# Kernel optimization log

Measured on AMD Instinct MI355X. Metric: run time of the kernel, lower is better.

The kernel has to match this reference:

```python
import jax, jax.numpy as jnp
import numpy as np

B = 16384          # batch size
NUM_NEG = 4
N = 1 + NUM_NEG    # items per row (pos + negs)
D = 128            # embedding_dim
F = 4              # num_factors
FS = D // F        # factor_size = 32
TD = 384           # bert_text_dim
NU = 100000        # num_users
NI = 100000        # num_items
HID = 150          # text MLP hidden
M = 2              # num_modalities


def _linear_init(k, fan_out, fan_in):
    bound = 1.0 / np.sqrt(fan_in)
    return jax.random.uniform(k, (fan_out, fan_in), jnp.float32, -bound, bound)


def setup_inputs() -> dict:
    key = jax.random.key(0)
    ks = jax.random.split(key, 12)
    batch = jax.random.randint(ks[0], (B, 1 + N), 0, NU)          # col0=user, cols1..5=items
    text = jax.random.normal(ks[1], (B, N, TD), dtype=jnp.float32)
    user_table = jax.random.normal(ks[2], (NU, D), dtype=jnp.float32)
    item_table = jax.random.normal(ks[3], (NI, D), dtype=jnp.float32)
    w1 = _linear_init(ks[4], HID, TD)
    b1 = jax.random.uniform(ks[5], (HID,), jnp.float32, -1/np.sqrt(TD), 1/np.sqrt(TD))
    w2 = _linear_init(ks[6], D, HID)
    b2 = jax.random.uniform(ks[7], (D,), jnp.float32, -1/np.sqrt(HID), 1/np.sqrt(HID))
    # per-factor attention MLPs, stacked over the F factors (all same size here)
    aw1 = jax.random.uniform(ks[8], (F, M, 3 * FS), jnp.float32, -1/np.sqrt(3*FS), 1/np.sqrt(3*FS))
    ab1 = jax.random.uniform(ks[9], (F, M), jnp.float32, -1/np.sqrt(3*FS), 1/np.sqrt(3*FS))
    aw2 = jax.random.uniform(ks[10], (F, M, M), jnp.float32, -1/np.sqrt(M), 1/np.sqrt(M))
    return dict(batch=batch, text=text, user_table=user_table, item_table=item_table,
                w1=w1, b1=b1, w2=w2, b2=b2, aw1=aw1, ab1=ab1, aw2=aw2)


def _leaky_relu(x):
    return jnp.where(x > 0, x, 0.01 * x)


def reference(batch, text, user_table, item_table, w1, b1, w2, b2, aw1, ab1, aw2):
    # text MLP: Linear -> LeakyReLU -> Linear -> LeakyReLU
    te = _leaky_relu(_leaky_relu(text @ w1.T + b1) @ w2.T + b2)   # [B,N,D]

    users = batch[:, 0]
    items = batch[:, 1:]
    u = user_table[users]                                          # [B,D]
    ie = item_table[items]                                         # [B,N,D]

    # split into F factors of size FS (vectorized over factor dim)
    uf = jnp.broadcast_to(u[:, None, :], ie.shape).reshape(B, N, F, FS)
    itf = ie.reshape(B, N, F, FS)
    tf = te.reshape(B, N, F, FS)

    cat = jnp.concatenate([uf, itf, tf], axis=-1)                  # [B,N,F,3*FS]
    nrm = jnp.linalg.norm(cat, axis=-1, keepdims=True)
    cat = cat / jnp.maximum(nrm, 1e-12)                            # F.normalize(dim=-1)

    h = jnp.tanh(jnp.einsum('bnfk,fmk->bnfm', cat, aw1) + ab1)     # [B,N,F,M]
    logits = jnp.einsum('bnfm,fom->bnfo', h, aw2)                  # [B,N,F,M]
    # torch nn.Softmax() with dim=None on a 3D tensor -> softmax over dim 0 (batch)
    attn = jax.nn.softmax(logits, axis=0)

    r_ui = attn[..., 0] * jax.nn.softplus(jnp.sum(uf * itf, axis=-1))  # [B,N,F]
    r_ut = attn[..., 1] * jax.nn.softplus(jnp.sum(uf * tf, axis=-1))   # [B,N,F]
    ratings = jnp.sum(r_ui + r_ut, axis=-1)                        # [B,N], sum over factors
    return ratings
```

## Files before the change

### kernel.cpp

```cpp
#include <hip/hip_runtime.h>
#include <hip/hip_bf16.h>

#define TDIM 384
#define HID 150
#define DD 128
#define ROWS 81920
#define RT 64

typedef __attribute__((ext_vector_type(8))) short short8;
typedef __attribute__((ext_vector_type(4))) float f32x4;

#define SMEM_BYTES 33792

__device__ __forceinline__ float lrelu(float x) { return x > 0.f ? x : 0.01f * x; }
__device__ __forceinline__ float softplusf(float x) {
    return fmaxf(x, 0.f) + log1pf(expf(-fabsf(x)));
}

__device__ __forceinline__ short8 pack8(const float4 a, const float4 b) {
    union { short8 s; __hip_bfloat16 h[8]; } u;
    u.h[0] = __float2bfloat16(a.x); u.h[1] = __float2bfloat16(a.y);
    u.h[2] = __float2bfloat16(a.z); u.h[3] = __float2bfloat16(a.w);
    u.h[4] = __float2bfloat16(b.x); u.h[5] = __float2bfloat16(b.y);
    u.h[6] = __float2bfloat16(b.z); u.h[7] = __float2bfloat16(b.w);
    return u.s;
}

__global__ __launch_bounds__(256)
void prep_w(const float* __restrict__ w1, const float* __restrict__ w2,
            short8* __restrict__ w1f, short8* __restrict__ w2f)
{
    const int idx = blockIdx.x * 256 + threadIdx.x;
    union { short8 s; __hip_bfloat16 h[8]; } u;
    if (idx < 7680) {
        const int kt = idx / 640, c = idx % 640;
        const int col = c >> 2, q = c & 3;
        const int k = kt * 32 + q * 8;
#pragma unroll
        for (int j = 0; j < 8; ++j)
            u.h[j] = __float2bfloat16(col < HID ? w1[(size_t)col * TDIM + k + j] : 0.f);
        w1f[idx] = u.s;
    } else if (idx < 10240) {
        const int i2 = idx - 7680;
        const int kt = i2 / 512, c = i2 % 512;
        const int col = c >> 2, q = c & 3;
        const int k = kt * 32 + q * 8;
#pragma unroll
        for (int j = 0; j < 8; ++j)
            u.h[j] = __float2bfloat16((k + j) < HID ? w2[(size_t)col * HID + k + j] : 0.f);
        w2f[i2] = u.s;
    }
}

__global__ __launch_bounds__(256, 4)
void fused_main(const int* __restrict__ batch,
                const float* __restrict__ text,
                const float* __restrict__ user_table,
                const float* __restrict__ item_table,
                const short8* __restrict__ w1f,
                const float* __restrict__ b1,
                const short8* __restrict__ w2f,
                const float* __restrict__ b2,
                const float* __restrict__ aw1,
                const float* __restrict__ ab1,
                const float* __restrict__ aw2,
                float* __restrict__ expp,
                float* __restrict__ Sglob)
{
    __shared__ __align__(16) unsigned char smem[SMEM_BYTES];
    __shared__ __align__(8) float red[512];
    __hip_bfloat16* Hs = (__hip_bfloat16*)(smem);
    float*          Ts = (float*)(smem);

    const int t    = threadIdx.x;
    const int r0   = blockIdx.x * RT;
    const int lane = t & 63;
    const int wv   = t >> 6;
    const int m16  = lane & 15;
    const int quad = lane >> 4;
    const int wr   = (wv & 1) * 32;
    const int wc   = (wv >> 1) * 80;
    const int wc2  = (wv >> 1) * 64;

    const int p3row = t >> 2;
    const int p3f   = t & 3;
    const int gr    = r0 + p3row;
    const int bb    = gr / 5;
    const int nn    = gr - bb * 5;
    const int uid   = batch[bb * 6];
    const int iid   = batch[bb * 6 + 1 + nn];

    const float* ta  = text + (size_t)(r0 + wr + m16) * TDIM;
    const float* tb  = ta + 16 * TDIM;
    const int    ko0 = quad * 8;
    const int w1base = (wc + m16) * 4 + quad;

    f32x4 acc1[2][5];
#pragma unroll
    for (int i = 0; i < 2; ++i)
#pragma unroll
        for (int j = 0; j < 5; ++j) acc1[i][j] = (f32x4){0.f, 0.f, 0.f, 0.f};

    float4 pA[2][4];
#pragma unroll
    for (int k = 0; k < 2; ++k) {
        pA[k][0] = *(const float4*)(ta + k * 32 + ko0);
        pA[k][1] = *(const float4*)(ta + k * 32 + ko0 + 4);
        pA[k][2] = *(const float4*)(tb + k * 32 + ko0);
        pA[k][3] = *(const float4*)(tb + k * 32 + ko0 + 4);
    }

#pragma unroll
    for (int kt = 0; kt < 12; ++kt) {
        const int p = kt & 1;
        short8 bw[5];
#pragma unroll
        for (int tj = 0; tj < 5; ++tj)
            bw[tj] = w1f[kt * 640 + w1base + tj * 64];
        const short8 a0 = pack8(pA[p][0], pA[p][1]);
        const short8 a1 = pack8(pA[p][2], pA[p][3]);
        if (kt < 10) {
            const int ko = (kt + 2) * 32 + ko0;
            pA[p][0] = *(const float4*)(ta + ko);
            pA[p][1] = *(const float4*)(ta + ko + 4);
            pA[p][2] = *(const float4*)(tb + ko);
            pA[p][3] = *(const float4*)(tb + ko + 4);
        }
#pragma unroll
        for (int tj = 0; tj < 5; ++tj) {
            acc1[0][tj] = __builtin_amdgcn_mfma_f32_16x16x32_bf16(a0, bw[tj], acc1[0][tj], 0, 0, 0);
            acc1[1][tj] = __builtin_amdgcn_mfma_f32_16x16x32_bf16(a1, bw[tj], acc1[1][tj], 0, 0, 0);
        }
    }

#pragma unroll
    for (int tj = 0; tj < 5; ++tj) {
        const int col = wc + tj * 16 + m16;
        const float bv = (col < HID) ? b1[col] : 0.f;
#pragma unroll
        for (int ti = 0; ti < 2; ++ti) {
#pragma unroll
            for (int r = 0; r < 4; ++r) {
                const int row = wr + ti * 16 + quad * 4 + r;
                float v = lrelu(acc1[ti][tj][r] + bv);
                if (col >= HID) v = 0.f;
                Hs[row * 168 + col] = __float2bfloat16(v);
            }
        }
    }
    __syncthreads();

    f32x4 acc2[2][4];
#pragma unroll
    for (int i = 0; i < 2; ++i)
#pragma unroll
        for (int j = 0; j < 4; ++j) acc2[i][j] = (f32x4){0.f, 0.f, 0.f, 0.f};

    const __hip_bfloat16* h0p = Hs + (wr + m16) * 168 + ko0;
    const __hip_bfloat16* h1p = h0p + 16 * 168;
    const int w2base = (wc2 + m16) * 4 + quad;

#pragma unroll
    for (int kt = 0; kt < 5; ++kt) {
        short8 bw[4];
#pragma unroll
        for (int tj = 0; tj < 4; ++tj)
            bw[tj] = w2f[kt * 512 + w2base + tj * 64];
        const short8 a0 = *(const short8*)(h0p + kt * 32);
        const short8 a1 = *(const short8*)(h1p + kt * 32);
#pragma unroll
        for (int tj = 0; tj < 4; ++tj) {
            acc2[0][tj] = __builtin_amdgcn_mfma_f32_16x16x32_bf16(a0, bw[tj], acc2[0][tj], 0, 0, 0);
            acc2[1][tj] = __builtin_amdgcn_mfma_f32_16x16x32_bf16(a1, bw[tj], acc2[1][tj], 0, 0, 0);
        }
    }
    __syncthreads();

#pragma unroll
    for (int tj = 0; tj < 4; ++tj) {
        const int col = wc2 + tj * 16 + m16;
        const float bv = b2[col];
#pragma unroll
        for (int ti = 0; ti < 2; ++ti) {
#pragma unroll
            for (int r = 0; r < 4; ++r) {
                const int row = wr + ti * 16 + quad * 4 + r;
                Ts[row * 132 + col] = lrelu(acc2[ti][tj][r] + bv);
            }
        }
    }

    const float* up = user_table + (size_t)uid * DD + p3f * 32;
    const float* ip = item_table + (size_t)iid * DD + p3f * 32;
    float4 ur[8], er[8];
#pragma unroll
    for (int q = 0; q < 8; ++q) {
        ur[q] = *(const float4*)(up + q * 4);
        er[q] = *(const float4*)(ip + q * 4);
    }
    __syncthreads();

    {
        const float* tp  = Ts + p3row * 132 + p3f * 32;
        const float* a1p = aw1 + p3f * 2 * 96;

        float ss = 0.f, z0 = 0.f, z1 = 0.f, sui = 0.f, sut = 0.f;
#pragma unroll
        for (int q = 0; q < 8; ++q) {
            const float4 u4 = ur[q];
            const float4 e4 = er[q];
            const float4 t4 = *(const float4*)(tp + q * 4);
            const float4 a00 = *(const float4*)(a1p + q * 4);
            const float4 a01 = *(const float4*)(a1p + 32 + q * 4);
            const float4 a02 = *(const float4*)(a1p + 64 + q * 4);
            const float4 a10 = *(const float4*)(a1p + 96 + q * 4);
            const float4 a11 = *(const float4*)(a1p + 128 + q * 4);
            const float4 a12 = *(const float4*)(a1p + 160 + q * 4);
            const float uu[4] = {u4.x, u4.y, u4.z, u4.w};
            const float ee[4] = {e4.x, e4.y, e4.z, e4.w};
            const float tt[4] = {t4.x, t4.y, t4.z, t4.w};
            const float w00[4] = {a00.x, a00.y, a00.z, a00.w};
            const float w01[4] = {a01.x, a01.y, a01.z, a01.w};
            const float w02[4] = {a02.x, a02.y, a02.z, a02.w};
            const float w10[4] = {a10.x, a10.y, a10.z, a10.w};
            const float w11[4] = {a11.x, a11.y, a11.z, a11.w};
            const float w12[4] = {a12.x, a12.y, a12.z, a12.w};
#pragma unroll
            for (int c = 0; c < 4; ++c) {
                const float u = uu[c], e = ee[c], x = tt[c];
                ss  = fmaf(u, u, ss); ss = fmaf(e, e, ss); ss = fmaf(x, x, ss);
                z0  = fmaf(u, w00[c], z0);
                z0  = fmaf(e, w01[c], z0);
                z0  = fmaf(x, w02[c], z0);
                z1  = fmaf(u, w10[c], z1);
                z1  = fmaf(e, w11[c], z1);
                z1  = fmaf(x, w12[c], z1);
                sui = fmaf(u, e, sui);
                sut = fmaf(u, x, sut);
            }
        }
        const float inv = 1.f / fmaxf(sqrtf(ss), 1e-12f);
        const float h0 = tanhf(fmaf(z0, inv, ab1[p3f * 2 + 0]));
        const float h1 = tanhf(fmaf(z1, inv, ab1[p3f * 2 + 1]));
        const float l0 = fmaf(h0, aw2[p3f * 4 + 0], h1 * aw2[p3f * 4 + 1]);
        const float l1 = fmaf(h0, aw2[p3f * 4 + 2], h1 * aw2[p3f * 4 + 3]);
        const float e0 = expf(l0), e1 = expf(l1);
        const float pui = softplusf(sui), put = softplusf(sut);
        *(float4*)&expp[((size_t)gr * 4 + p3f) * 4] = make_float4(e0, e1, pui, put);
        *(float2*)&red[p3row * 8 + p3f * 2] = make_float2(e0, e1);
    }
    __syncthreads();

    if (t < 40) {
        const int j   = t & 7;
        const int nn0 = t >> 3;
        int r = nn0 - (r0 % 5);
        if (r < 0) r += 5;
        float s = 0.f;
        for (; r < RT; r += 5) s += red[r * 8 + j];
        atomicAdd(&Sglob[t * 32], s);
    }
}

__global__ void finalize(const float* __restrict__ expp,
                         const float* __restrict__ Sglob,
                         float* __restrict__ out)
{
    const int gr = blockIdx.x * 256 + threadIdx.x;
    if (gr >= ROWS) return;
    const int b = gr / 5;
    const int n = gr - b * 5;
    float r = 0.f;
#pragma unroll
    for (int f = 0; f < 4; ++f) {
        const float4 v = *(const float4*)&expp[((size_t)gr * 4 + f) * 4];
        const float S0 = Sglob[(n * 8 + f * 2 + 0) * 32];
        const float S1 = Sglob[(n * 8 + f * 2 + 1) * 32];
        r += v.x / S0 * v.z + v.y / S1 * v.w;
    }
    out[gr] = r;
}

extern "C" void kernel_launch(void* const* d_in, const int* in_sizes, int n_in,
                              void* d_out, int out_size, void* d_ws, size_t ws_size,
                              hipStream_t stream)
{
    (void)in_sizes; (void)n_in; (void)out_size; (void)ws_size;
    const int*   batch      = (const int*)d_in[0];
    const float* text       = (const float*)d_in[1];
    const float* user_table = (const float*)d_in[2];
    const float* item_table = (const float*)d_in[3];
    const float* w1         = (const float*)d_in[4];
    const float* b1         = (const float*)d_in[5];
    const float* w2         = (const float*)d_in[6];
    const float* b2         = (const float*)d_in[7];
    const float* aw1        = (const float*)d_in[8];
    const float* ab1        = (const float*)d_in[9];
    const float* aw2        = (const float*)d_in[10];
    float* out = (float*)d_out;

    char* ws = (char*)d_ws;
    short8* w1f   = (short8*)ws;
    short8* w2f   = (short8*)(ws + 122880);
    float*  expp  = (float*)(ws + 163840);
    float*  Sglob = (float*)(ws + 163840 + (size_t)ROWS * 16 * 4);

    hipMemsetAsync(Sglob, 0, 40 * 32 * sizeof(float), stream);
    prep_w<<<40, 256, 0, stream>>>(w1, w2, w1f, w2f);
    fused_main<<<ROWS / RT, 256, 0, stream>>>(batch, text, user_table, item_table,
                                              w1f, b1, w2f, b2, aw1, ab1, aw2,
                                              expp, Sglob);
    finalize<<<(ROWS + 255) / 256, 256, 0, stream>>>(expp, Sglob, out);
}
```

Before: 352.2 us.

## Halve row tile, split per-factor work across lane pairs, replicate atomic sums

Shrinks the row tile from 64 to 32 so each wave does one 16-row MFMA strip, which halves accumulator registers and shared memory and raises launch bounds to 8 blocks per CU. The per-factor attention stage is split across two lanes per factor and combined with xor shuffles, so the 256 threads cover the smaller tile. Softmax denominator atomics are spread over 8 replicas to reduce contention, and finalize now reduces those replicas once into shared memory. The trade-off is twice as many blocks, with more redundant weight-fragment loads per row and more atomics overall.

```diff
diff --git a/kernel.cpp b/kernel.cpp
--- a/kernel.cpp
+++ b/kernel.cpp
@@ -5,12 +5,12 @@
 #define HID 150
 #define DD 128
 #define ROWS 81920
-#define RT 64
+#define RT 32
 
 typedef __attribute__((ext_vector_type(8))) short short8;
 typedef __attribute__((ext_vector_type(4))) float f32x4;
 
-#define SMEM_BYTES 33792
+#define SMEM_BYTES 16896
 
 __device__ __forceinline__ float lrelu(float x) { return x > 0.f ? x : 0.01f * x; }
 __device__ __forceinline__ float softplusf(float x) {
@@ -52,7 +52,7 @@
     }
 }
 
-__global__ __launch_bounds__(256, 4)
+__global__ __launch_bounds__(256, 8)
 void fused_main(const int* __restrict__ batch,
                 const float* __restrict__ text,
                 const float* __restrict__ user_table,
@@ -68,7 +68,7 @@
                 float* __restrict__ Sglob)
 {
     __shared__ __align__(16) unsigned char smem[SMEM_BYTES];
-    __shared__ __align__(8) float red[512];
+    __shared__ __align__(8) float red[RT * 8];
     __hip_bfloat16* Hs = (__hip_bfloat16*)(smem);
     float*          Ts = (float*)(smem);
 
@@ -78,36 +78,30 @@
     const int wv   = t >> 6;
     const int m16  = lane & 15;
     const int quad = lane >> 4;
-    const int wr   = (wv & 1) * 32;
+    const int wr   = (wv & 1) * 16;
     const int wc   = (wv >> 1) * 80;
     const int wc2  = (wv >> 1) * 64;
 
-    const int p3row = t >> 2;
-    const int p3f   = t & 3;
+    const int p3row = t >> 3;
+    const int p3f   = (t >> 1) & 3;
+    const int half  = t & 1;
     const int gr    = r0 + p3row;
     const int bb    = gr / 5;
     const int nn    = gr - bb * 5;
-    const int uid   = batch[bb * 6];
-    const int iid   = batch[bb * 6 + 1 + nn];
 
     const float* ta  = text + (size_t)(r0 + wr + m16) * TDIM;
-    const float* tb  = ta + 16 * TDIM;
     const int    ko0 = quad * 8;
     const int w1base = (wc + m16) * 4 + quad;
 
-    f32x4 acc1[2][5];
-#pragma unroll
-    for (int i = 0; i < 2; ++i)
-#pragma unroll
-        for (int j = 0; j < 5; ++j) acc1[i][j] = (f32x4){0.f, 0.f, 0.f, 0.f};
-
-    float4 pA[2][4];
+    f32x4 acc1[5];
+#pragma unroll
+    for (int j = 0; j < 5; ++j) acc1[j] = (f32x4){0.f, 0.f, 0.f, 0.f};
+
+    float4 pA[2][2];
 #pragma unroll
     for (int k = 0; k < 2; ++k) {
         pA[k][0] = *(const float4*)(ta + k * 32 + ko0);
         pA[k][1] = *(const float4*)(ta + k * 32 + ko0 + 4);
-        pA[k][2] = *(const float4*)(tb + k * 32 + ko0);
-        pA[k][3] = *(const float4*)(tb + k * 32 + ko0 + 4);
     }
 
 #pragma unroll
@@ -118,19 +112,14 @@
         for (int tj = 0; tj < 5; ++tj)
             bw[tj] = w1f[kt * 640 + w1base + tj * 64];
         const short8 a0 = pack8(pA[p][0], pA[p][1]);
-        const short8 a1 = pack8(pA[p][2], pA[p][3]);
         if (kt < 10) {
             const int ko = (kt + 2) * 32 + ko0;
             pA[p][0] = *(const float4*)(ta + ko);
             pA[p][1] = *(const float4*)(ta + ko + 4);
-            pA[p][2] = *(const float4*)(tb + ko);
-            pA[p][3] = *(const float4*)(tb + ko + 4);
-        }
-#pragma unroll
-        for (int tj = 0; tj < 5; ++tj) {
-            acc1[0][tj] = __builtin_amdgcn_mfma_f32_16x16x32_bf16(a0, bw[tj], acc1[0][tj], 0, 0, 0);
-            acc1[1][tj] = __builtin_amdgcn_mfma_f32_16x16x32_bf16(a1, bw[tj], acc1[1][tj], 0, 0, 0);
-        }
+        }
+#pragma unroll
+        for (int tj = 0; tj < 5; ++tj)
+            acc1[tj] = __builtin_amdgcn_mfma_f32_16x16x32_bf16(a0, bw[tj], acc1[tj], 0, 0, 0);
     }
 
 #pragma unroll
@@ -138,26 +127,20 @@
         const int col = wc + tj * 16 + m16;
         const float bv = (col < HID) ? b1[col] : 0.f;
 #pragma unroll
-        for (int ti = 0; ti < 2; ++ti) {
-#pragma unroll
-            for (int r = 0; r < 4; ++r) {
-                const int row = wr + ti * 16 + quad * 4 + r;
-                float v = lrelu(acc1[ti][tj][r] + bv);
-                if (col >= HID) v = 0.f;
-                Hs[row * 168 + col] = __float2bfloat16(v);
-            }
-        }
-    }
-    __syncthreads();
-
-    f32x4 acc2[2][4];
-#pragma unroll
-    for (int i = 0; i < 2; ++i)
-#pragma unroll
-        for (int j = 0; j < 4; ++j) acc2[i][j] = (f32x4){0.f, 0.f, 0.f, 0.f};
+        for (int r = 0; r < 4; ++r) {
+            const int row = wr + quad * 4 + r;
+            float v = lrelu(acc1[tj][r] + bv);
+            if (col >= HID) v = 0.f;
+            Hs[row * 168 + col] = __float2bfloat16(v);
+        }
+    }
+    __syncthreads();
+
+    f32x4 acc2[4];
+#pragma unroll
+    for (int j = 0; j < 4; ++j) acc2[j] = (f32x4){0.f, 0.f, 0.f, 0.f};
 
     const __hip_bfloat16* h0p = Hs + (wr + m16) * 168 + ko0;
-    const __hip_bfloat16* h1p = h0p + 16 * 168;
     const int w2base = (wc2 + m16) * 4 + quad;
 
 #pragma unroll
@@ -167,12 +150,9 @@
         for (int tj = 0; tj < 4; ++tj)
             bw[tj] = w2f[kt * 512 + w2base + tj * 64];
         const short8 a0 = *(const short8*)(h0p + kt * 32);
-        const short8 a1 = *(const short8*)(h1p + kt * 32);
-#pragma unroll
-        for (int tj = 0; tj < 4; ++tj) {
-            acc2[0][tj] = __builtin_amdgcn_mfma_f32_16x16x32_bf16(a0, bw[tj], acc2[0][tj], 0, 0, 0);
-            acc2[1][tj] = __builtin_amdgcn_mfma_f32_16x16x32_bf16(a1, bw[tj], acc2[1][tj], 0, 0, 0);
-        }
+#pragma unroll
+        for (int tj = 0; tj < 4; ++tj)
+            acc2[tj] = __builtin_amdgcn_mfma_f32_16x16x32_bf16(a0, bw[tj], acc2[tj], 0, 0, 0);
     }
     __syncthreads();
 
@@ -181,32 +161,31 @@
         const int col = wc2 + tj * 16 + m16;
         const float bv = b2[col];
 #pragma unroll
-        for (int ti = 0; ti < 2; ++ti) {
-#pragma unroll
-            for (int r = 0; r < 4; ++r) {
-                const int row = wr + ti * 16 + quad * 4 + r;
-                Ts[row * 132 + col] = lrelu(acc2[ti][tj][r] + bv);
-            }
-        }
-    }
-
-    const float* up = user_table + (size_t)uid * DD + p3f * 32;
-    const float* ip = item_table + (size_t)iid * DD + p3f * 32;
-    float4 ur[8], er[8];
-#pragma unroll
-    for (int q = 0; q < 8; ++q) {
+        for (int r = 0; r < 4; ++r) {
+            const int row = wr + quad * 4 + r;
+            Ts[row * 132 + col] = lrelu(acc2[tj][r] + bv);
+        }
+    }
+
+    const int uid = batch[bb * 6];
+    const int iid = batch[bb * 6 + 1 + nn];
+    const float* up = user_table + (size_t)uid * DD + p3f * 32 + half * 16;
+    const float* ip = item_table + (size_t)iid * DD + p3f * 32 + half * 16;
+    float4 ur[4], er[4];
+#pragma unroll
+    for (int q = 0; q < 4; ++q) {
         ur[q] = *(const float4*)(up + q * 4);
         er[q] = *(const float4*)(ip + q * 4);
     }
     __syncthreads();
 
     {
-        const float* tp  = Ts + p3row * 132 + p3f * 32;
-        const float* a1p = aw1 + p3f * 2 * 96;
+        const float* tp  = Ts + p3row * 132 + p3f * 32 + half * 16;
+        const float* a1p = aw1 + p3f * 192 + half * 16;
 
         float ss = 0.f, z0 = 0.f, z1 = 0.f, sui = 0.f, sut = 0.f;
 #pragma unroll
-        for (int q = 0; q < 8; ++q) {
+        for (int q = 0; q < 4; ++q) {
             const float4 u4 = ur[q];
             const float4 e4 = er[q];
             const float4 t4 = *(const float4*)(tp + q * 4);
@@ -239,6 +218,12 @@
                 sut = fmaf(u, x, sut);
             }
         }
+        ss  += __shfl_xor(ss, 1);
+        z0  += __shfl_xor(z0, 1);
+        z1  += __shfl_xor(z1, 1);
+        sui += __shfl_xor(sui, 1);
+        sut += __shfl_xor(sut, 1);
+
         const float inv = 1.f / fmaxf(sqrtf(ss), 1e-12f);
         const float h0 = tanhf(fmaf(z0, inv, ab1[p3f * 2 + 0]));
         const float h1 = tanhf(fmaf(z1, inv, ab1[p3f * 2 + 1]));
@@ -246,36 +231,53 @@
         const float l1 = fmaf(h0, aw2[p3f * 4 + 2], h1 * aw2[p3f * 4 + 3]);
         const float e0 = expf(l0), e1 = expf(l1);
         const float pui = softplusf(sui), put = softplusf(sut);
-        *(float4*)&expp[((size_t)gr * 4 + p3f) * 4] = make_float4(e0, e1, pui, put);
-        *(float2*)&red[p3row * 8 + p3f * 2] = make_float2(e0, e1);
+        if (half == 0) {
+            *(float4*)&expp[((size_t)gr * 4 + p3f) * 4] = make_float4(e0, e1, pui, put);
+            *(float2*)&red[p3row * 8 + p3f * 2] = make_float2(e0, e1);
+        }
     }
     __syncthreads();
 
     if (t < 40) {
         const int j   = t & 7;
         const int nn0 = t >> 3;
+        const int rep = blockIdx.x & 7;
         int r = nn0 - (r0 % 5);
         if (r < 0) r += 5;
         float s = 0.f;
         for (; r < RT; r += 5) s += red[r * 8 + j];
-        atomicAdd(&Sglob[t * 32], s);
-    }
-}
-
-__global__ void finalize(const float* __restrict__ expp,
-                         const float* __restrict__ Sglob,
-                         float* __restrict__ out)
+        atomicAdd(&Sglob[((t * 8) + rep) * 16], s);
+    }
+}
+
+__global__ __launch_bounds__(256)
+void finalize(const float* __restrict__ expp,
+              const float* __restrict__ Sglob,
+              float* __restrict__ out)
 {
-    const int gr = blockIdx.x * 256 + threadIdx.x;
-    if (gr >= ROWS) return;
+    __shared__ float Ss[40];
+    const int t = threadIdx.x;
+
+    if (t < 160) {
+        const int cidx = t >> 2;
+        const int rp   = t & 3;
+        float v = Sglob[(cidx * 8 + rp * 2 + 0) * 16]
+                + Sglob[(cidx * 8 + rp * 2 + 1) * 16];
+        v += __shfl_xor(v, 1);
+        v += __shfl_xor(v, 2);
+        if (rp == 0) Ss[cidx] = v;
+    }
+    __syncthreads();
+
+    const int gr = blockIdx.x * 256 + t;
     const int b = gr / 5;
     const int n = gr - b * 5;
     float r = 0.f;
 #pragma unroll
     for (int f = 0; f < 4; ++f) {
         const float4 v = *(const float4*)&expp[((size_t)gr * 4 + f) * 4];
-        const float S0 = Sglob[(n * 8 + f * 2 + 0) * 32];
-        const float S1 = Sglob[(n * 8 + f * 2 + 1) * 32];
+        const float S0 = Ss[n * 8 + f * 2 + 0];
+        const float S1 = Ss[n * 8 + f * 2 + 1];
         r += v.x / S0 * v.z + v.y / S1 * v.w;
     }
     out[gr] = r;
@@ -305,10 +307,10 @@
     float*  expp  = (float*)(ws + 163840);
     float*  Sglob = (float*)(ws + 163840 + (size_t)ROWS * 16 * 4);
 
-    hipMemsetAsync(Sglob, 0, 40 * 32 * sizeof(float), stream);
+    hipMemsetAsync(Sglob, 0, 320 * 16 * sizeof(float), stream);
     prep_w<<<40, 256, 0, stream>>>(w1, w2, w1f, w2f);
     fused_main<<<ROWS / RT, 256, 0, stream>>>(batch, text, user_table, item_table,
                                               w1f, b1, w2f, b2, aw1, ab1, aw2,
                                               expp, Sglob);
-    finalize<<<(ROWS + 255) / 256, 256, 0, stream>>>(expp, Sglob, out);
-}
+    finalize<<<ROWS / 256, 256, 0, stream>>>(expp, Sglob, out);
+}
```

Result: faster. 334.6 us (-5.0%).
